# Kernel tuning notes

Hardware: AMD Instinct MI355X
Metric: run time of the kernel (lower is better)

The kernel has to match this reference:

```python
import jax, jax.numpy as jnp
import numpy as np

B, S, K = 128, 1024, 256


def setup_inputs() -> dict:
    key = jax.random.key(0)
    k1, k2, k3, k4, k5 = jax.random.split(key, 5)
    emissions = jax.random.normal(k1, (B, S, K), dtype=jnp.float32)
    targets = jax.random.randint(k2, (B, S), 0, K)
    masks = jnp.ones((B, S), dtype=bool)
    start_transitions = jax.random.uniform(k3, (K,), minval=-0.1, maxval=0.1, dtype=jnp.float32)
    end_transitions = jax.random.uniform(k4, (K,), minval=-0.1, maxval=0.1, dtype=jnp.float32)
    transitions = jax.random.uniform(k5, (K, K), minval=-0.1, maxval=0.1, dtype=jnp.float32)
    return {
        "emissions": emissions,
        "targets": targets,
        "masks": masks,
        "start_transitions": start_transitions,
        "end_transitions": end_transitions,
        "transitions": transitions,
    }


def reference(emissions, targets, masks, start_transitions, end_transitions, transitions):
    # batch_first=True -> transpose to time-major (S, B, ...)
    em = jnp.swapaxes(emissions, 0, 1)            # (S, B, K)
    tgt = jnp.swapaxes(targets, 0, 1)             # (S, B)
    msk = jnp.swapaxes(masks, 0, 1)               # (S, B) bool
    mf = msk.astype(em.dtype)
    batch_idx = jnp.arange(em.shape[1])

    # ---- numerator: gold path score ----
    em_t = jnp.take_along_axis(em, tgt[:, :, None], axis=2)[:, :, 0]   # (S, B)
    trans_t = transitions[tgt[:-1], tgt[1:]]                            # (S-1, B)
    numerator = start_transitions[tgt[0]] + em_t[0]
    numerator = numerator + jnp.sum((trans_t + em_t[1:]) * mf[1:], axis=0)
    seq_ends = msk.astype(jnp.int32).sum(axis=0) - 1                    # (B,)
    last_tags = tgt[seq_ends, batch_idx]
    numerator = numerator + end_transitions[last_tags]

    # ---- denominator: log partition via forward scan ----
    def step(score, inp):
        e_i, m_i = inp  # (B, K), (B,)
        # (B, K_prev, 1) + (K_prev, K_next) + (B, 1, K_next) -> logsumexp over prev
        nxt = jax.nn.logsumexp(score[:, :, None] + transitions[None, :, :] + e_i[:, None, :], axis=1)
        score = jnp.where(m_i[:, None], nxt, score)
        return score, None

    score0 = start_transitions[None, :] + em[0]                         # (B, K)
    score, _ = jax.lax.scan(step, score0, (em[1:], msk[1:]))
    denominator = jax.nn.logsumexp(score + end_transitions[None, :], axis=1)

    return numerator - denominator  # (B,) log-likelihood per sequence
```

## Files before the change

### kernel.cpp

```cpp
#include <hip/hip_runtime.h>
#include <hip/hip_fp16.h>

#define CRF_S 1024
#define CRF_K 256

typedef _Float16 half2_t __attribute__((ext_vector_type(2)));
typedef _Float16 half8_t __attribute__((ext_vector_type(8)));

__device__ __forceinline__ float wave_reduce_max(float v) {
#pragma unroll
  for (int off = 32; off > 0; off >>= 1) v = fmaxf(v, __shfl_xor(v, off));
  return v;
}
__device__ __forceinline__ float wave_reduce_sum(float v) {
#pragma unroll
  for (int off = 32; off > 0; off >>= 1) v += __shfl_xor(v, off);
  return v;
}

#if defined(__has_builtin)
#if __has_builtin(__builtin_amdgcn_fdot2)
#define HAVE_FDOT2 1
#endif
#endif

__device__ __forceinline__ float dot2_acc(half2_t a, half2_t b, float c) {
#ifdef HAVE_FDOT2
  return __builtin_amdgcn_fdot2(a, b, c, false);
#else
  return c + (float)a[0] * (float)b[0] + (float)a[1] * (float)b[1];
#endif
}

__global__ __launch_bounds__(1024) void crf_fused(
    const float* __restrict__ em, const int* __restrict__ tgt,
    const float* __restrict__ startT, const float* __restrict__ endT,
    const float* __restrict__ trans, float* __restrict__ out) {
  __shared__ __align__(16) _Float16 pbuf[2][288];
  __shared__ float abuf[2];
  __shared__ float fin[48];

  const int b = blockIdx.x, tid = threadIdx.x;
  const int j = tid >> 2, q = tid & 3;
  const int lane = tid & 63, wv = tid >> 6;
  const float* emb = em + (size_t)b * CRF_S * CRF_K;
  const int* tb = tgt + (size_t)b * CRF_S;

  half2_t ereg[32];
#pragma unroll
  for (int c = 0; c < 32; ++c) {
    float t0 = trans[(q * 64 + 2 * c) * CRF_K + j];
    float t1 = trans[(q * 64 + 2 * c + 1) * CRF_K + j];
    half2_t u;
    u[0] = (_Float16)__expf(t0);
    u[1] = (_Float16)__expf(t1);
    ereg[c] = u;
  }

  float nacc = 0.f;
  if (tid >= 1) nacc = trans[tb[tid - 1] * CRF_K + tb[tid]] + emb[(size_t)tid * CRF_K + tb[tid]];
  nacc = wave_reduce_sum(nacc);
  if (lane == 0) fin[32 + wv] = nacc;

  float score = startT[j] + emb[j];
  if (tid == 0) abuf[0] = score;
  __syncthreads();
  float anch = abuf[0];

  float numer = 0.f;
  if (tid == 0) {
    float a = 0.f;
#pragma unroll
    for (int w = 0; w < 16; ++w) a += fin[32 + w];
    numer = startT[tb[0]] + emb[tb[0]] + a + endT[tb[CRF_S - 1]];
  }

  const float C = 8.3177661667f;
  const int pskew = j + ((j >> 6) << 3);
  const _Float16* pbase0 = &pbuf[0][q * 72];
  const _Float16* pbase1 = &pbuf[1][q * 72];

  float em_c = emb[CRF_K + j];
  float em_n = emb[2 * CRF_K + j];

#define CRF_STEP(T_IDX, PAR)                                                   \
  {                                                                            \
    float em_f = ((T_IDX) + 2 < CRF_S)                                         \
                     ? emb[(size_t)((T_IDX) + 2) * CRF_K + j]                  \
                     : 0.f;                                                    \
    float x = fminf(score - anch - C, 11.0f);                                  \
    float p = __expf(x);                                                       \
    if (q == 0) pbuf[PAR][pskew] = (_Float16)p;                                \
    __syncthreads();                                                           \
    float a_new = abuf[(PAR) ^ 1];            \
    const _Float16* pb = (PAR) ? pbase1 : pbase0;                              \
    float d0 = 0.f, d1 = 0.f, d2 = 0.f, d3 = 0.f;                              \
    _Pragma("unroll") for (int c2 = 0; c2 < 8; ++c2) {                         \
      half8_t p8 = *(const half8_t*)(pb + c2 * 8); \
      d0 = dot2_acc(ereg[4 * c2 + 0], (half2_t){p8[0], p8[1]}, d0);            \
      d1 = dot2_acc(ereg[4 * c2 + 1], (half2_t){p8[2], p8[3]}, d1);            \
      d2 = dot2_acc(ereg[4 * c2 + 2], (half2_t){p8[4], p8[5]}, d2);            \
      d3 = dot2_acc(ereg[4 * c2 + 3], (half2_t){p8[6], p8[7]}, d3);            \
    }                                                                          \
    float dt = (d0 + d1) + (d2 + d3);                                          \
    dt += __shfl_xor(dt, 1);                    \
    dt += __shfl_xor(dt, 2);                                                   \
    score = anch + C + em_c + __logf(dt);                                      \
    if (tid == 0) abuf[PAR] = score;                                           \
    anch = a_new;                                                              \
    em_c = em_n;                                                               \
    em_n = em_f;                                                               \
  }

  for (int t = 1; t < CRF_S - 1; t += 2) {
    CRF_STEP(t, 1);
    CRF_STEP(t + 1, 0);
  }
  CRF_STEP(CRF_S - 1, 1);
#undef CRF_STEP

  float v = score + endT[j];
  float wmx = wave_reduce_max(v);
  if (lane == 0) fin[wv] = wmx;
  __syncthreads();
  float m = fin[0];
#pragma unroll
  for (int w = 1; w < 16; ++w) m = fmaxf(m, fin[w]);
  float pe = 0.25f * __expf(v - m);
  float ws = wave_reduce_sum(pe);
  if (lane == 0) fin[16 + wv] = ws;
  __syncthreads();
  if (tid == 0) {
    float S = 0.f;
#pragma unroll
    for (int w = 0; w < 16; ++w) S += fin[16 + w];
    out[b] = numer - (m + __logf(S));
  }
}

extern "C" void kernel_launch(void* const* d_in, const int* in_sizes, int n_in,
                              void* d_out, int out_size, void* d_ws, size_t ws_size,
                              hipStream_t stream) {
  const float* em = (const float*)d_in[0];
  const int* tgt = (const int*)d_in[1];
  const float* startT = (const float*)d_in[3];
  const float* endT = (const float*)d_in[4];
  const float* trans = (const float*)d_in[5];
  float* out = (float*)d_out;

  const int B = in_sizes[1] / CRF_S;
  crf_fused<<<B, 1024, 0, stream>>>(em, tgt, startT, endT, trans, out);
}
```

Measured before the change: 852.2 us.

## Restructure CRF forward scan into 16-lane groups with scaled-probability recurrence

Each group of 16 threads now computes four output states, with each lane covering 16 predecessors, and the partial dot products are reduced with DPP row shifts instead of cross-lane shuffles. The scan now carries scaled probabilities in fp16 shared memory plus a running log-normalizer L. This removes the per-step log/exp round trip and the max/logsumexp in the epilogue, and emissions are loaded as float4. The rescaling anchor is the log of state 0's probability, and values are clamped to fp16 range, which risks overflow or underflow and accuracy loss if state 0 becomes very unlikely.

```diff
diff --git a/kernel.cpp b/kernel.cpp
--- a/kernel.cpp
+++ b/kernel.cpp
@@ -5,13 +5,10 @@
 #define CRF_K 256
 
 typedef _Float16 half2_t __attribute__((ext_vector_type(2)));
+typedef _Float16 half4_t __attribute__((ext_vector_type(4)));
 typedef _Float16 half8_t __attribute__((ext_vector_type(8)));
+typedef float float4_t __attribute__((ext_vector_type(4)));
 
-__device__ __forceinline__ float wave_reduce_max(float v) {
-#pragma unroll
-  for (int off = 32; off > 0; off >>= 1) v = fmaxf(v, __shfl_xor(v, off));
-  return v;
-}
 __device__ __forceinline__ float wave_reduce_sum(float v) {
 #pragma unroll
   for (int off = 32; off > 0; off >>= 1) v += __shfl_xor(v, off);
@@ -32,82 +29,124 @@
 #endif
 }
 
-__global__ __launch_bounds__(1024) void crf_fused(
+__device__ __forceinline__ float row16_sum(float v) {
+  v += __int_as_float(__builtin_amdgcn_update_dpp(0, __float_as_int(v), 0x121, 0xf, 0xf, true));
+  v += __int_as_float(__builtin_amdgcn_update_dpp(0, __float_as_int(v), 0x122, 0xf, 0xf, true));
+  v += __int_as_float(__builtin_amdgcn_update_dpp(0, __float_as_int(v), 0x124, 0xf, 0xf, true));
+  v += __int_as_float(__builtin_amdgcn_update_dpp(0, __float_as_int(v), 0x128, 0xf, 0xf, true));
+  return v;
+}
+
+__global__ __launch_bounds__(1024, 4) void crf_fused(
     const float* __restrict__ em, const int* __restrict__ tgt,
     const float* __restrict__ startT, const float* __restrict__ endT,
     const float* __restrict__ trans, float* __restrict__ out) {
-  __shared__ __align__(16) _Float16 pbuf[2][288];
+  __shared__ __align__(16) _Float16 pbuf[2][16 * 24];
   __shared__ float abuf[2];
-  __shared__ float fin[48];
+  __shared__ float fin[32];
 
   const int b = blockIdx.x, tid = threadIdx.x;
-  const int j = tid >> 2, q = tid & 3;
+  const int sg = tid >> 4, q = tid & 15;
+  const int sg4 = sg << 2;
   const int lane = tid & 63, wv = tid >> 6;
   const float* emb = em + (size_t)b * CRF_S * CRF_K;
   const int* tb = tgt + (size_t)b * CRF_S;
-
-  half2_t ereg[32];
-#pragma unroll
-  for (int c = 0; c < 32; ++c) {
-    float t0 = trans[(q * 64 + 2 * c) * CRF_K + j];
-    float t1 = trans[(q * 64 + 2 * c + 1) * CRF_K + j];
-    half2_t u;
-    u[0] = (_Float16)__expf(t0);
-    u[1] = (_Float16)__expf(t1);
-    ereg[c] = u;
-  }
+  const float C = 8.3177661667f;
 
   float nacc = 0.f;
   if (tid >= 1) nacc = trans[tb[tid - 1] * CRF_K + tb[tid]] + emb[(size_t)tid * CRF_K + tb[tid]];
   nacc = wave_reduce_sum(nacc);
-  if (lane == 0) fin[32 + wv] = nacc;
+  if (lane == 0) fin[16 + wv] = nacc;
 
-  float score = startT[j] + emb[j];
-  if (tid == 0) abuf[0] = score;
+  half2_t u[4][8];
+#pragma unroll
+  for (int k = 0; k < 8; ++k) {
+    float4_t ra = *(const float4_t*)(trans + (16 * q + 2 * k) * CRF_K + sg4);
+    float4_t rb = *(const float4_t*)(trans + (16 * q + 2 * k + 1) * CRF_K + sg4);
+#pragma unroll
+    for (int c = 0; c < 4; ++c) {
+      half2_t h;
+      h[0] = (_Float16)__expf(ra[c]);
+      h[1] = (_Float16)__expf(rb[c]);
+      u[c][k] = h;
+    }
+  }
+
+  float4_t st4 = *(const float4_t*)(startT + sg4);
+  float4_t em0 = *(const float4_t*)(emb + sg4);
+  float s00_pub = st4[0] + em0[0];
+  if (tid == 0) abuf[1] = s00_pub;
   __syncthreads();
-  float anch = abuf[0];
+  float a0 = abuf[1];
+  float L = a0 + C;
 
   float numer = 0.f;
   if (tid == 0) {
     float a = 0.f;
 #pragma unroll
-    for (int w = 0; w < 16; ++w) a += fin[32 + w];
+    for (int w = 0; w < 16; ++w) a += fin[16 + w];
     numer = startT[tb[0]] + emb[tb[0]] + a + endT[tb[CRF_S - 1]];
   }
 
-  const float C = 8.3177661667f;
-  const int pskew = j + ((j >> 6) << 3);
-  const _Float16* pbase0 = &pbuf[0][q * 72];
-  const _Float16* pbase1 = &pbuf[1][q * 72];
+  const int widx = (sg >> 2) * 24 + (sg4 & 15);
+  {
+    float p0[4];
+#pragma unroll
+    for (int c = 0; c < 4; ++c) p0[c] = __expf(fminf(st4[c] + em0[c] - a0 - C, 11.f));
+    if (q == 0) {
+      half4_t pk;
+#pragma unroll
+      for (int c = 0; c < 4; ++c) pk[c] = (_Float16)p0[c];
+      *(half4_t*)(&pbuf[0][widx]) = pk;
+    }
+    if (tid == 0) abuf[0] = __logf(p0[0]);
+  }
 
-  float em_c = emb[CRF_K + j];
-  float em_n = emb[2 * CRF_K + j];
+  float4_t em_c = *(const float4_t*)(emb + CRF_K + sg4);
+  float4_t em_n = *(const float4_t*)(emb + 2 * CRF_K + sg4);
+  const float4_t zero4 = {0.f, 0.f, 0.f, 0.f};
 
 #define CRF_STEP(T_IDX, PAR)                                                   \
   {                                                                            \
-    float em_f = ((T_IDX) + 2 < CRF_S)                                         \
-                     ? emb[(size_t)((T_IDX) + 2) * CRF_K + j]                  \
-                     : 0.f;                                                    \
-    float x = fminf(score - anch - C, 11.0f);                                  \
-    float p = __expf(x);                                                       \
-    if (q == 0) pbuf[PAR][pskew] = (_Float16)p;                                \
-    __syncthreads();                                                           \
-    float a_new = abuf[(PAR) ^ 1];            \
-    const _Float16* pb = (PAR) ? pbase1 : pbase0;                              \
+    __syncthreads();             \
+    float mu = abuf[(PAR) ^ 1] + C;                                            \
+    const _Float16* pb = &pbuf[(PAR) ^ 1][q * 24];                             \
+    half8_t pa = *(const half8_t*)(pb);                                        \
+    half8_t pz = *(const half8_t*)(pb + 8);                                    \
+    float4_t em_f = zero4;                                                     \
+    if ((T_IDX) + 2 < CRF_S)                                                   \
+      em_f = *(const float4_t*)(emb + (size_t)((T_IDX) + 2) * CRF_K + sg4);    \
     float d0 = 0.f, d1 = 0.f, d2 = 0.f, d3 = 0.f;                              \
-    _Pragma("unroll") for (int c2 = 0; c2 < 8; ++c2) {                         \
-      half8_t p8 = *(const half8_t*)(pb + c2 * 8); \
-      d0 = dot2_acc(ereg[4 * c2 + 0], (half2_t){p8[0], p8[1]}, d0);            \
-      d1 = dot2_acc(ereg[4 * c2 + 1], (half2_t){p8[2], p8[3]}, d1);            \
-      d2 = dot2_acc(ereg[4 * c2 + 2], (half2_t){p8[4], p8[5]}, d2);            \
-      d3 = dot2_acc(ereg[4 * c2 + 3], (half2_t){p8[6], p8[7]}, d3);            \
+    _Pragma("unroll") for (int k = 0; k < 4; ++k) {                            \
+      half2_t pk = {pa[2 * k], pa[2 * k + 1]};                                 \
+      d0 = dot2_acc(u[0][k], pk, d0);                                          \
+      d1 = dot2_acc(u[1][k], pk, d1);                                          \
+      d2 = dot2_acc(u[2][k], pk, d2);                                          \
+      d3 = dot2_acc(u[3][k], pk, d3);                                          \
     }                                                                          \
-    float dt = (d0 + d1) + (d2 + d3);                                          \
-    dt += __shfl_xor(dt, 1);                    \
-    dt += __shfl_xor(dt, 2);                                                   \
-    score = anch + C + em_c + __logf(dt);                                      \
-    if (tid == 0) abuf[PAR] = score;                                           \
-    anch = a_new;                                                              \
+    _Pragma("unroll") for (int k = 0; k < 4; ++k) {                            \
+      half2_t pk = {pz[2 * k], pz[2 * k + 1]};                                 \
+      d0 = dot2_acc(u[0][k + 4], pk, d0);                                      \
+      d1 = dot2_acc(u[1][k + 4], pk, d1);                                      \
+      d2 = dot2_acc(u[2][k + 4], pk, d2);                                      \
+      d3 = dot2_acc(u[3][k + 4], pk, d3);                                      \
+    }                                                                          \
+    d0 = row16_sum(d0);                                                        \
+    d1 = row16_sum(d1);                                                        \
+    d2 = row16_sum(d2);                                                        \
+    d3 = row16_sum(d3);                                                        \
+    L += mu;                                                                   \
+    float p0v = fminf(d0 * __expf(em_c[0] - mu), 60000.f);                     \
+    float p1v = fminf(d1 * __expf(em_c[1] - mu), 60000.f);                     \
+    float p2v = fminf(d2 * __expf(em_c[2] - mu), 60000.f);                     \
+    float p3v = fminf(d3 * __expf(em_c[3] - mu), 60000.f);                     \
+    if (q == 0) {                                                              \
+      half4_t pk;                                                              \
+      pk[0] = (_Float16)p0v; pk[1] = (_Float16)p1v;                            \
+      pk[2] = (_Float16)p2v; pk[3] = (_Float16)p3v;                            \
+      *(half4_t*)(&pbuf[PAR][widx]) = pk;                                      \
+    }                                                                          \
+    if (tid == 0) abuf[PAR] = __logf(p0v);                                     \
     em_c = em_n;                                                               \
     em_n = em_f;                                                               \
   }
@@ -119,22 +158,22 @@
   CRF_STEP(CRF_S - 1, 1);
 #undef CRF_STEP
 
-  float v = score + endT[j];
-  float wmx = wave_reduce_max(v);
-  if (lane == 0) fin[wv] = wmx;
   __syncthreads();
-  float m = fin[0];
-#pragma unroll
-  for (int w = 1; w < 16; ++w) m = fmaxf(m, fin[w]);
-  float pe = 0.25f * __expf(v - m);
-  float ws = wave_reduce_sum(pe);
-  if (lane == 0) fin[16 + wv] = ws;
+  float spart = 0.f;
+  if (q == 0) {
+    half4_t pf = *(const half4_t*)(&pbuf[1][widx]);
+    float4_t e4 = *(const float4_t*)(endT + sg4);
+    spart = (float)pf[0] * __expf(e4[0]) + (float)pf[1] * __expf(e4[1]) +
+            (float)pf[2] * __expf(e4[2]) + (float)pf[3] * __expf(e4[3]);
+  }
+  spart = wave_reduce_sum(spart);
+  if (lane == 0) fin[wv] = spart;
   __syncthreads();
   if (tid == 0) {
     float S = 0.f;
 #pragma unroll
-    for (int w = 0; w < 16; ++w) S += fin[16 + w];
-    out[b] = numer - (m + __logf(S));
+    for (int w = 0; w < 16; ++w) S += fin[w];
+    out[b] = numer - (L + __logf(S));
   }
 }
 
```

New measurement: 884.6 us. 1.04x slower.
